# Optimization experiments

Measured on AMD Instinct MI355X. Metric: run time of the kernel, lower is better.

## Reference

```python
import math
import jax, jax.numpy as jnp
import numpy as np

B, T, D, H = 4, 2048, 1024, 16
DH = D // H


def setup_inputs() -> dict:
    key = jax.random.key(0)
    ks = jax.random.split(key, 12)
    s = 1.0 / math.sqrt(D)
    return {
        "query": jax.random.normal(ks[0], (B, T, D), jnp.float32),
        "key": jax.random.normal(ks[1], (B, T, D), jnp.float32),
        "value": jax.random.normal(ks[2], (B, T, D), jnp.float32),
        "mask": jax.random.randint(ks[3], (1, 1, T, T), 0, 2).astype(jnp.bool_),
        "Wq": jax.random.normal(ks[4], (D, D), jnp.float32) * s,
        "bq": jnp.zeros((D,), jnp.float32),
        "Wk": jax.random.normal(ks[5], (D, D), jnp.float32) * s,
        "bk": jnp.zeros((D,), jnp.float32),
        "Wv": jax.random.normal(ks[6], (D, D), jnp.float32) * s,
        "bv": jnp.zeros((D,), jnp.float32),
        "Wo": jax.random.normal(ks[7], (D, D), jnp.float32) * s,
        "bo": jnp.zeros((D,), jnp.float32),
    }


def _heads(x):
    # [B,T,D] -> [B,H,T,DH]
    b, t, _ = x.shape
    return x.reshape(b, t, H, DH).transpose(0, 2, 1, 3)


def reference(query, key, value, mask, Wq, bq, Wk, bk, Wv, bv, Wo, bo):
    q = _heads(query @ Wq.T + bq)
    k = _heads(key @ Wk.T + bk)
    v = _heads(value @ Wv.T + bv)
    # NOTE: original scales by 1/sqrt(embed_dim), not head_dim
    logits = jnp.einsum('bhqd,bhkd->bhqk', q, k) / math.sqrt(D)
    logits = jnp.where(mask, -jnp.inf, logits)
    scores = jax.nn.softmax(logits, axis=-1)
    o = jnp.einsum('bhqk,bhkd->bhqd', scores, v)  # [B,H,T,DH]
    o = o.transpose(0, 2, 1, 3).reshape(query.shape[0], -1, D)
    return o @ Wo.T + bo
```

## Files before the change

kernel.cpp:

```cpp
#include <hip/hip_runtime.h>
#include <hip/hip_bf16.h>

#define D_MODEL 1024
#define SEQ     2048
#define BATCH   4
#define NH      16
#define DHEAD   64

typedef __attribute__((ext_vector_type(8))) short bhalf8;
typedef __attribute__((ext_vector_type(4))) float floatx4;
typedef __attribute__((ext_vector_type(16))) float floatx16;
typedef __attribute__((ext_vector_type(4))) unsigned int uintx4;
typedef __attribute__((ext_vector_type(2))) unsigned int uintx2;

__device__ __forceinline__ void gload16(const void* g, void* l) {
  __builtin_amdgcn_global_load_lds(
      (const __attribute__((address_space(1))) unsigned int*)g,
      (__attribute__((address_space(3))) unsigned int*)l, 16, 0, 0);
}

__device__ __forceinline__ unsigned short f2bf(float x) {
  __hip_bfloat16 h = __float2bfloat16(x);
  return __builtin_bit_cast(unsigned short, h);
}

__device__ __forceinline__ uintx2 pl32(unsigned int a, unsigned int b) {
  return __builtin_amdgcn_permlane32_swap(a, b, false, false);
}

__global__ void cvt_bf16_kernel(const float* __restrict__ in,
                                unsigned short* __restrict__ out, int n4) {
  int i = blockIdx.x * blockDim.x + threadIdx.x;
  if (i >= n4) return;
  float4 v = ((const float4*)in)[i];
  ushort4 o;
  o.x = f2bf(v.x); o.y = f2bf(v.y); o.z = f2bf(v.z); o.w = f2bf(v.w);
  ((ushort4*)out)[i] = o;
}

__global__ void cvt_all_kernel(const float* __restrict__ q, const float* __restrict__ k,
                               const float* __restrict__ v, const float* __restrict__ wq,
                               const float* __restrict__ wk, const float* __restrict__ wv,
                               const float* __restrict__ wo,
                               unsigned short* __restrict__ xq, unsigned short* __restrict__ xk,
                               unsigned short* __restrict__ xv, unsigned short* __restrict__ wqb,
                               unsigned short* __restrict__ wkb, unsigned short* __restrict__ wvb,
                               unsigned short* __restrict__ wob) {
  const int L = blockIdx.x;
  const float* src;
  unsigned short* dst;
  int base;
  if      (L < 8192)  { src = q;  dst = xq;  base = 0; }
  else if (L < 16384) { src = k;  dst = xk;  base = 8192; }
  else if (L < 24576) { src = v;  dst = xv;  base = 16384; }
  else if (L < 25600) { src = wq; dst = wqb; base = 24576; }
  else if (L < 26624) { src = wk; dst = wkb; base = 25600; }
  else if (L < 27648) { src = wv; dst = wvb; base = 26624; }
  else                { src = wo; dst = wob; base = 27648; }
  const int i = (L - base) * 256 + threadIdx.x;
  float4 vv = ((const float4*)src)[i];
  ushort4 o;
  o.x = f2bf(vv.x); o.y = f2bf(vv.y); o.z = f2bf(vv.z); o.w = f2bf(vv.w);
  ((ushort4*)dst)[i] = o;
}

__global__ void detect_mask_kernel(const unsigned int* __restrict__ m,
                                   unsigned int* __restrict__ flag) {
  __shared__ unsigned int not_int, not_flt;
  if (threadIdx.x == 0) { not_int = 0u; not_flt = 0u; }
  __syncthreads();
  unsigned int ni = 0u, nf = 0u;
  for (int j = 0; j < 4; ++j) {
    unsigned int w = m[threadIdx.x * 4 + j];
    if (w > 1u) ni = 1u;
    if (w != 0u && w != 0x3f800000u) nf = 1u;
  }
  if (ni) atomicOr(&not_int, 1u);
  if (nf) atomicOr(&not_flt, 1u);
  __syncthreads();
  if (threadIdx.x == 0) {
    unsigned int f = 1u;
    if (!not_int) f = 0u;
    else if (!not_flt) f = 2u;
    *flag = f;
  }
}

__global__ void pack_mask_kernel(const void* __restrict__ mraw,
                                 const unsigned int* __restrict__ flag,
                                 unsigned long long* __restrict__ bits) {
  int t = blockIdx.x * blockDim.x + threadIdx.x;
  unsigned int f = *flag;
  int v;
  if (f == 1u) v = (((const unsigned char*)mraw)[t] != 0);
  else         v = (((const unsigned int*)mraw)[t] != 0u);
  unsigned long long b = __ballot(v == 0);
  if ((threadIdx.x & 63) == 0) bits[t >> 6] = b;
}

template <int F32OUT>
__device__ __forceinline__ void gemm_core(const unsigned short* __restrict__ A,
                                          const unsigned short* __restrict__ B,
                                          const float* __restrict__ bias,
                                          void* __restrict__ Cout,
                                          int N, float scale, int biasM, int L) {
  __shared__ unsigned short As[2][128][64];
  __shared__ unsigned short Bs[2][128][64];
  const int tid = threadIdx.x;
  const int wid = tid >> 6, lane = tid & 63;
  const int g = lane >> 4, c = lane & 15;
  const int wr = wid >> 1, wc = wid & 1;

  const int xcd = L & 7;
  const int i5 = L >> 3;
  const int u = i5 & 7, v5 = i5 >> 3;
  int bx, by;
  if ((N >> 7) == 8) { bx = u; by = xcd + 8 * v5; }
  else               { bx = xcd + 8 * u; by = v5; }
  const int m0 = by * 128, n0 = bx * 128;

  const floatx4 zero4 = {0.f, 0.f, 0.f, 0.f};
  floatx4 acc[4][4];
#pragma unroll
  for (int i = 0; i < 4; ++i)
#pragma unroll
    for (int j = 0; j < 4; ++j) acc[i][j] = zero4;

  const int r_ = tid >> 3;
  const int sb = ((tid & 7) * 16) ^ (((tid >> 3) & 7) << 4);
  const char* Asrc = (const char*)(A + (size_t)(m0 + r_) * 1024) + sb;
  const char* Bsrc = (const char*)(B + (size_t)(n0 + r_) * 1024) + sb;
  const size_t ROWP = (size_t)32 * 1024 * 2;

  auto stage = [&](int kt, int buf) {
    const size_t ko = (size_t)kt * 128;
#pragma unroll
    for (int p = 0; p < 4; ++p) {
      gload16(Asrc + ko + p * ROWP, (char*)&As[buf][0][0] + p * 4096 + tid * 16);
      gload16(Bsrc + ko + p * ROWP, (char*)&Bs[buf][0][0] + p * 4096 + tid * 16);
    }
  };

  stage(0, 0);
  __syncthreads();
  int cur = 0;
  for (int kt = 0; kt < 16; ++kt) {
    if (kt + 1 < 16) stage(kt + 1, cur ^ 1);
    const char* abase = (const char*)&As[cur][0][0];
    const char* bbase = (const char*)&Bs[cur][0][0];
    bhalf8 a[2][4], b[2][4];
#pragma unroll
    for (int kk = 0; kk < 2; ++kk) {
#pragma unroll
      for (int i = 0; i < 4; ++i) {
        const int row = wr * 64 + i * 16 + c;
        a[kk][i] = *(const bhalf8*)(abase + row * 128 +
                                    ((kk * 64 + g * 16) ^ ((row & 7) << 4)));
      }
#pragma unroll
      for (int j = 0; j < 4; ++j) {
        const int row = wc * 64 + j * 16 + c;
        b[kk][j] = *(const bhalf8*)(bbase + row * 128 +
                                    ((kk * 64 + g * 16) ^ ((row & 7) << 4)));
      }
    }
#pragma unroll
    for (int kk = 0; kk < 2; ++kk)
#pragma unroll
      for (int i = 0; i < 4; ++i)
#pragma unroll
        for (int j = 0; j < 4; ++j)
          acc[i][j] = __builtin_amdgcn_mfma_f32_16x16x32_bf16(a[kk][i], b[kk][j], acc[i][j], 0, 0, 0);
    __syncthreads();
    cur ^= 1;
  }

  float bn[4] = {0.f, 0.f, 0.f, 0.f};
  if (!biasM) {
#pragma unroll
    for (int j = 0; j < 4; ++j) bn[j] = bias[n0 + wc * 64 + j * 16 + c];
  }
#pragma unroll
  for (int i = 0; i < 4; ++i) {
    float bm[4] = {0.f, 0.f, 0.f, 0.f};
    if (biasM) {
#pragma unroll
      for (int r = 0; r < 4; ++r) bm[r] = bias[m0 + wr * 64 + i * 16 + 4 * g + r];
    }
#pragma unroll
    for (int j = 0; j < 4; ++j) {
#pragma unroll
      for (int r = 0; r < 4; ++r) {
        const int m = m0 + wr * 64 + i * 16 + 4 * g + r;
        const int n = n0 + wc * 64 + j * 16 + c;
        const float v = (acc[i][j][r] + (biasM ? bm[r] : bn[j])) * scale;
        if (F32OUT) ((float*)Cout)[(size_t)m * N + n] = v;
        else ((unsigned short*)Cout)[(size_t)m * N + n] = f2bf(v);
      }
    }
  }
}

__global__ __launch_bounds__(256, 2)
void gemm_qkv_kernel(const unsigned short* __restrict__ Xq,
                     const unsigned short* __restrict__ Xk,
                     const unsigned short* __restrict__ Xv,
                     const unsigned short* __restrict__ Wqb,
                     const unsigned short* __restrict__ Wkb,
                     const unsigned short* __restrict__ Wvb,
                     const float* __restrict__ bq, const float* __restrict__ bk,
                     const float* __restrict__ bv,
                     unsigned short* __restrict__ Qb, unsigned short* __restrict__ Kb,
                     unsigned short* __restrict__ Vtb, float qscale, int jsel) {
  int j, L;
  if (jsel == 3) { j = blockIdx.x >> 9; L = blockIdx.x & 511; }
  else           { j = jsel; L = blockIdx.x; }
  const unsigned short* A = (j == 0) ? Xq : (j == 1) ? Xk : Wvb;
  const unsigned short* B = (j == 0) ? Wqb : (j == 1) ? Wkb : Xv;
  const float* bias = (j == 0) ? bq : (j == 1) ? bk : bv;
  unsigned short* C = (j == 0) ? Qb : (j == 1) ? Kb : Vtb;
  const int N = (j == 2) ? 8192 : 1024;
  const float scale = (j == 0) ? qscale : 1.0f;
  gemm_core<0>(A, B, bias, C, N, scale, (j == 2) ? 1 : 0, L);
}

__global__ __launch_bounds__(256, 2)
void gemm_out_kernel(const unsigned short* __restrict__ A,
                     const unsigned short* __restrict__ B,
                     const float* __restrict__ bias, float* __restrict__ C) {
  gemm_core<1>(A, B, bias, C, 1024, 1.0f, 0, blockIdx.x);
}

__global__ __launch_bounds__(256, 3)
void attn_kernel(const unsigned short* __restrict__ Q,
                 const unsigned short* __restrict__ Kmat,
                 const unsigned short* __restrict__ Vt,
                 const unsigned long long* __restrict__ mbits,
                 unsigned short* __restrict__ O) {
  __shared__ unsigned short Ks[2][64][64];
  __shared__ unsigned short Vs[2][64][64];

  const int tid = threadIdx.x;
  const int wid = tid >> 6, lane = tid & 63;
  const int ql = lane & 31;
  const int hi = lane >> 5;

  const int L = blockIdx.x;
  const int xcd = L & 7;
  const int s = L >> 3;
  const int bh = (s & 7) * 8 + xcd;
  const int qt = s >> 3;
  const int b = bh >> 4, h = bh & 15;
  const int q0 = qt * 128 + wid * 32;

  const unsigned short* Qb = Q + (size_t)(b * SEQ + q0) * D_MODEL + h * DHEAD;
  const unsigned short* Kb = Kmat + (size_t)(b * SEQ) * D_MODEL + h * DHEAD;
  const unsigned short* Vb = Vt + (size_t)(h * DHEAD) * (BATCH * SEQ) + (size_t)b * SEQ;

  bhalf8 qf[4];
#pragma unroll
  for (int ks = 0; ks < 4; ++ks)
    qf[ks] = *(const bhalf8*)(Qb + (size_t)ql * D_MODEL + ks * 16 + hi * 8);

  const floatx16 z16 = {0,0,0,0,0,0,0,0,0,0,0,0,0,0,0,0};
  floatx16 ot[2];
  ot[0] = z16; ot[1] = z16;
  floatx16 lt = z16;

  const short ONEB = (short)0x3F80;
  const bhalf8 ones8 = {ONEB, ONEB, ONEB, ONEB, ONEB, ONEB, ONEB, ONEB};

  int koff[4];
#pragma unroll
  for (int ks = 0; ks < 4; ++ks)
    koff[ks] = ql * 128 + ((ks * 32 + hi * 16) ^ ((ql & 7) << 4));

  const int sr = tid >> 3;
  const int sbz = ((tid & 7) * 16) ^ ((sr & 7) << 4);
  const char* Ksrc = (const char*)(Kb + (size_t)sr * D_MODEL) + sbz;
  const char* Vsrc = (const char*)(Vb + (size_t)sr * (BATCH * SEQ)) + sbz;
  const size_t KR32 = (size_t)32 * D_MODEL * 2;
  const size_t VR32 = (size_t)32 * (BATCH * SEQ) * 2;
  const size_t KSTEP = (size_t)64 * D_MODEL * 2;
  const size_t VSTEP = 128;

  const int NT = SEQ / 64;
  gload16(Ksrc,        (char*)&Ks[0][0][0] + tid * 16);
  gload16(Ksrc + KR32, (char*)&Ks[0][0][0] + 4096 + tid * 16);
  gload16(Vsrc,        (char*)&Vs[0][0][0] + tid * 16);
  gload16(Vsrc + VR32, (char*)&Vs[0][0][0] + 4096 + tid * 16);
  __syncthreads();
  const char* kp = Ksrc + KSTEP;
  const char* vp = Vsrc + VSTEP;
  const unsigned long long* mp = mbits + (size_t)(q0 + ql) * (SEQ / 64);
  int cur = 0;

  for (int kt = 0; kt < NT; ++kt) {
    if (kt + 1 < NT) {
      gload16(kp,        (char*)&Ks[cur ^ 1][0][0] + tid * 16);
      gload16(kp + KR32, (char*)&Ks[cur ^ 1][0][0] + 4096 + tid * 16);
      gload16(vp,        (char*)&Vs[cur ^ 1][0][0] + tid * 16);
      gload16(vp + VR32, (char*)&Vs[cur ^ 1][0][0] + 4096 + tid * 16);
      kp += KSTEP;
      vp += VSTEP;
    }
    const unsigned long long mws = mp[kt] >> (4 * hi);
    const unsigned int mlo = (unsigned int)mws;
    const unsigned int mhi32 = (unsigned int)(mws >> 32);

    const char* kbase = (const char*)&Ks[cur][0][0];
    const char* vbase = (const char*)&Vs[cur][0][0];

    floatx16 st[2];
    __builtin_amdgcn_s_setprio(1);
#pragma unroll
    for (int blk = 0; blk < 2; ++blk) {
      const bhalf8 kf0 = *(const bhalf8*)(kbase + koff[0] + blk * 4096);
      st[blk] = __builtin_amdgcn_mfma_f32_32x32x16_bf16(kf0, qf[0], z16, 0, 0, 0);
    }
#pragma unroll
    for (int ks = 1; ks < 4; ++ks) {
#pragma unroll
      for (int blk = 0; blk < 2; ++blk) {
        const bhalf8 kf = *(const bhalf8*)(kbase + koff[ks] + blk * 4096);
        st[blk] = __builtin_amdgcn_mfma_f32_32x32x16_bf16(kf, qf[ks], st[blk], 0, 0, 0);
      }
    }
    __builtin_amdgcn_s_setprio(0);

    unsigned int w[2][8];
#pragma unroll
    for (int blk = 0; blk < 2; ++blk) {
      const unsigned int word = blk ? mhi32 : mlo;
#pragma unroll
      for (int i = 0; i < 8; ++i) {
        const int r0 = 2 * i, r1 = 2 * i + 1;
        const int c0 = (r0 & 3) + 8 * (r0 >> 2);
        const int c1 = c0 + 1;
        float p0 = __builtin_amdgcn_exp2f(st[blk][r0]);
        float p1 = __builtin_amdgcn_exp2f(st[blk][r1]);
        const unsigned int e0 = (unsigned int)__builtin_amdgcn_sbfe((int)word, c0, 1);
        const unsigned int e1 = (unsigned int)__builtin_amdgcn_sbfe((int)word, c1, 1);
        p0 = __builtin_bit_cast(float, __builtin_bit_cast(unsigned int, p0) & e0);
        p1 = __builtin_bit_cast(float, __builtin_bit_cast(unsigned int, p1) & e1);
        w[blk][i] = ((unsigned int)f2bf(p1) << 16) | (unsigned int)f2bf(p0);
      }
    }

    __builtin_amdgcn_s_setprio(1);
#pragma unroll
    for (int blk = 0; blk < 2; ++blk)
#pragma unroll
      for (int s2 = 0; s2 < 2; ++s2) {
        const int ks = blk * 2 + s2;
        const int o = s2 * 4;
        const uintx2 u2 = pl32(w[blk][o + 0], w[blk][o + 2]);
        const uintx2 v2 = pl32(w[blk][o + 1], w[blk][o + 3]);
        uintx4 awv;
        awv[0] = u2[0];  awv[1] = v2[0];  awv[2] = u2[1];  awv[3] = v2[1];
        const bhalf8 pa = __builtin_bit_cast(bhalf8, awv);
#pragma unroll
        for (int db = 0; db < 2; ++db) {
          const bhalf8 vf = *(const bhalf8*)(vbase + koff[ks] + db * 4096);
          ot[db] = __builtin_amdgcn_mfma_f32_32x32x16_bf16(pa, vf, ot[db], 0, 0, 0);
        }
        lt = __builtin_amdgcn_mfma_f32_32x32x16_bf16(pa, ones8, lt, 0, 0, 0);
      }
    __builtin_amdgcn_s_setprio(0);

    __syncthreads();
    cur ^= 1;
  }

#pragma unroll
  for (int r = 0; r < 16; ++r) {
    const int qr = (r & 3) + 8 * (r >> 2) + 4 * hi;
    const float fi = 1.f / lt[r];
    unsigned short* orow = O + (size_t)(b * SEQ + q0 + qr) * D_MODEL + h * DHEAD + ql;
    orow[0]  = f2bf(ot[0][r] * fi);
    orow[32] = f2bf(ot[1][r] * fi);
  }
}

extern "C" void kernel_launch(void* const* d_in, const int* in_sizes, int n_in,
                              void* d_out, int out_size, void* d_ws, size_t ws_size,
                              hipStream_t stream) {
  (void)in_sizes; (void)n_in; (void)out_size;
  const float* query = (const float*)d_in[0];
  const float* key   = (const float*)d_in[1];
  const float* value = (const float*)d_in[2];
  const void*  mask  = d_in[3];
  const float* Wq = (const float*)d_in[4];
  const float* bq = (const float*)d_in[5];
  const float* Wk = (const float*)d_in[6];
  const float* bk = (const float*)d_in[7];
  const float* Wv = (const float*)d_in[8];
  const float* bv = (const float*)d_in[9];
  const float* Wo = (const float*)d_in[10];
  const float* bo = (const float*)d_in[11];

  const float QSCALE = 1.4426950408889634f / 32.0f;
  const size_t XB = (size_t)8192 * 1024 * 2;
  const size_t WB = (size_t)1024 * 1024 * 2;
  const size_t MB = (size_t)2048 * 32 * 8;

  char* ws = (char*)d_ws;
  size_t off = 0;
  auto alloc = [&](size_t bytes) {
    char* p = ws + off;
    off += (bytes + 255) & ~(size_t)255;
    return p;
  };

  {
    size_t o2 = 0;
    auto need = [&](size_t b) { o2 += (b + 255) & ~(size_t)255; };
    need(XB); need(XB); need(XB);
    need(WB); need(WB); need(WB); need(WB);
    need(XB); need(XB); need(XB);
    need(MB); need(256);
    if (o2 <= ws_size) {
      unsigned short* Xq  = (unsigned short*)alloc(XB);
      unsigned short* Xk  = (unsigned short*)alloc(XB);
      unsigned short* Xv  = (unsigned short*)alloc(XB);
      unsigned short* Wqb = (unsigned short*)alloc(WB);
      unsigned short* Wkb = (unsigned short*)alloc(WB);
      unsigned short* Wvb = (unsigned short*)alloc(WB);
      unsigned short* Wob = (unsigned short*)alloc(WB);
      unsigned short* Qb  = (unsigned short*)alloc(XB);
      unsigned short* Kbf = (unsigned short*)alloc(XB);
      unsigned short* Vtb = (unsigned short*)alloc(XB);
      unsigned long long* mbits = (unsigned long long*)alloc(MB);
      unsigned int* flag = (unsigned int*)alloc(256);
      unsigned short* Ob = Xq;

      detect_mask_kernel<<<1, 256, 0, stream>>>((const unsigned int*)mask, flag);
      pack_mask_kernel<<<(SEQ * SEQ) / 256, 256, 0, stream>>>(mask, flag, mbits);
      cvt_all_kernel<<<28672, 256, 0, stream>>>(query, key, value, Wq, Wk, Wv, Wo,
                                                Xq, Xk, Xv, Wqb, Wkb, Wvb, Wob);
      gemm_qkv_kernel<<<1536, 256, 0, stream>>>(Xq, Xk, Xv, Wqb, Wkb, Wvb,
                                                bq, bk, bv, Qb, Kbf, Vtb, QSCALE, 3);
      attn_kernel<<<1024, 256, 0, stream>>>(Qb, Kbf, Vtb, mbits, Ob);
      gemm_out_kernel<<<512, 256, 0, stream>>>(Ob, Wob, bo, (float*)d_out);
      return;
    }
  }

  unsigned short* Xb  = (unsigned short*)alloc(XB);
  unsigned short* Wb  = (unsigned short*)alloc(WB);
  unsigned short* Qb  = (unsigned short*)alloc(XB);
  unsigned short* Kbf = (unsigned short*)alloc(XB);
  unsigned short* Vtb = (unsigned short*)alloc(XB);
  unsigned short* Ob  = (unsigned short*)alloc(XB);
  unsigned long long* mbits = (unsigned long long*)alloc(MB);
  unsigned int* flag = (unsigned int*)alloc(256);
  if (off > ws_size) return;

  detect_mask_kernel<<<1, 256, 0, stream>>>((const unsigned int*)mask, flag);
  pack_mask_kernel<<<(SEQ * SEQ) / 256, 256, 0, stream>>>(mask, flag, mbits);

  cvt_bf16_kernel<<<8192, 256, 0, stream>>>(query, Xb, 2097152);
  cvt_bf16_kernel<<<1024, 256, 0, stream>>>(Wq, Wb, 262144);
  gemm_qkv_kernel<<<512, 256, 0, stream>>>(Xb, Xb, Xb, Wb, Wb, Wb, bq, bk, bv,
                                           Qb, Kbf, Vtb, QSCALE, 0);
  cvt_bf16_kernel<<<8192, 256, 0, stream>>>(key, Xb, 2097152);
  cvt_bf16_kernel<<<1024, 256, 0, stream>>>(Wk, Wb, 262144);
  gemm_qkv_kernel<<<512, 256, 0, stream>>>(Xb, Xb, Xb, Wb, Wb, Wb, bq, bk, bv,
                                           Qb, Kbf, Vtb, QSCALE, 1);
  cvt_bf16_kernel<<<8192, 256, 0, stream>>>(value, Xb, 2097152);
  cvt_bf16_kernel<<<1024, 256, 0, stream>>>(Wv, Wb, 262144);
  gemm_qkv_kernel<<<512, 256, 0, stream>>>(Xb, Xb, Xb, Wb, Wb, Wb, bq, bk, bv,
                                           Qb, Kbf, Vtb, QSCALE, 2);
  attn_kernel<<<1024, 256, 0, stream>>>(Qb, Kbf, Vtb, mbits, Ob);
  cvt_bf16_kernel<<<1024, 256, 0, stream>>>(Wo, Wb, 262144);
  gemm_out_kernel<<<512, 256, 0, stream>>>(Ob, Wb, bo, (float*)d_out);
}
```

Measured before the change: 241.4 us.

## Enlarge attention block to 256 queries, widen conversion and mask packing per thread

The attention kernel now runs 512 threads (8 waves) per block over 256 query rows, so each K/V tile loaded into shared memory is shared by twice as many queries, and each thread issues one async load per tile instead of two. The grid shrinks to 512 blocks. The fp32-to-bf16 conversion kernel handles 8 elements per thread with 16-byte stores, and mask packing produces 8 ballot words per wave, which cuts launch and block overhead. The risks are lower occupancy, since 512 blocks gives fewer waves in flight per CU, and tail imbalance in the attention kernel.

```diff
diff --git a/kernel.cpp b/kernel.cpp
--- a/kernel.cpp
+++ b/kernel.cpp
@@ -12,6 +12,7 @@
 typedef __attribute__((ext_vector_type(16))) float floatx16;
 typedef __attribute__((ext_vector_type(4))) unsigned int uintx4;
 typedef __attribute__((ext_vector_type(2))) unsigned int uintx2;
+typedef __attribute__((ext_vector_type(8))) unsigned short ushort8v;
 
 __device__ __forceinline__ void gload16(const void* g, void* l) {
   __builtin_amdgcn_global_load_lds(
@@ -50,18 +51,20 @@
   const float* src;
   unsigned short* dst;
   int base;
-  if      (L < 8192)  { src = q;  dst = xq;  base = 0; }
-  else if (L < 16384) { src = k;  dst = xk;  base = 8192; }
-  else if (L < 24576) { src = v;  dst = xv;  base = 16384; }
-  else if (L < 25600) { src = wq; dst = wqb; base = 24576; }
-  else if (L < 26624) { src = wk; dst = wkb; base = 25600; }
-  else if (L < 27648) { src = wv; dst = wvb; base = 26624; }
-  else                { src = wo; dst = wob; base = 27648; }
+  if      (L < 4096)  { src = q;  dst = xq;  base = 0; }
+  else if (L < 8192)  { src = k;  dst = xk;  base = 4096; }
+  else if (L < 12288) { src = v;  dst = xv;  base = 8192; }
+  else if (L < 12800) { src = wq; dst = wqb; base = 12288; }
+  else if (L < 13312) { src = wk; dst = wkb; base = 12800; }
+  else if (L < 13824) { src = wv; dst = wvb; base = 13312; }
+  else                { src = wo; dst = wob; base = 13824; }
   const int i = (L - base) * 256 + threadIdx.x;
-  float4 vv = ((const float4*)src)[i];
-  ushort4 o;
-  o.x = f2bf(vv.x); o.y = f2bf(vv.y); o.z = f2bf(vv.z); o.w = f2bf(vv.w);
-  ((ushort4*)dst)[i] = o;
+  const float4 v0 = ((const float4*)src)[2 * i];
+  const float4 v1 = ((const float4*)src)[2 * i + 1];
+  ushort8v o;
+  o[0] = f2bf(v0.x); o[1] = f2bf(v0.y); o[2] = f2bf(v0.z); o[3] = f2bf(v0.w);
+  o[4] = f2bf(v1.x); o[5] = f2bf(v1.y); o[6] = f2bf(v1.z); o[7] = f2bf(v1.w);
+  ((ushort8v*)dst)[i] = o;
 }
 
 __global__ void detect_mask_kernel(const unsigned int* __restrict__ m,
@@ -89,13 +92,18 @@
 __global__ void pack_mask_kernel(const void* __restrict__ mraw,
                                  const unsigned int* __restrict__ flag,
                                  unsigned long long* __restrict__ bits) {
-  int t = blockIdx.x * blockDim.x + threadIdx.x;
-  unsigned int f = *flag;
-  int v;
-  if (f == 1u) v = (((const unsigned char*)mraw)[t] != 0);
-  else         v = (((const unsigned int*)mraw)[t] != 0u);
-  unsigned long long b = __ballot(v == 0);
-  if ((threadIdx.x & 63) == 0) bits[t >> 6] = b;
+  const unsigned int f = *flag;
+  const int lane = threadIdx.x & 63;
+  const int w0 = ((blockIdx.x * blockDim.x + threadIdx.x) >> 6) * 8;
+#pragma unroll
+  for (int e = 0; e < 8; ++e) {
+    const int t = (w0 + e) * 64 + lane;
+    int v;
+    if (f == 1u) v = (((const unsigned char*)mraw)[t] != 0);
+    else         v = (((const unsigned int*)mraw)[t] != 0u);
+    const unsigned long long b = __ballot(v == 0);
+    if (lane == 0) bits[w0 + e] = b;
+  }
 }
 
 template <int F32OUT>
@@ -231,7 +239,7 @@
   gemm_core<1>(A, B, bias, C, 1024, 1.0f, 0, blockIdx.x);
 }
 
-__global__ __launch_bounds__(256, 3)
+__global__ __launch_bounds__(512, 2)
 void attn_kernel(const unsigned short* __restrict__ Q,
                  const unsigned short* __restrict__ Kmat,
                  const unsigned short* __restrict__ Vt,
@@ -251,7 +259,7 @@
   const int bh = (s & 7) * 8 + xcd;
   const int qt = s >> 3;
   const int b = bh >> 4, h = bh & 15;
-  const int q0 = qt * 128 + wid * 32;
+  const int q0 = qt * 256 + wid * 32;
 
   const unsigned short* Qb = Q + (size_t)(b * SEQ + q0) * D_MODEL + h * DHEAD;
   const unsigned short* Kb = Kmat + (size_t)(b * SEQ) * D_MODEL + h * DHEAD;
@@ -279,16 +287,12 @@
   const int sbz = ((tid & 7) * 16) ^ ((sr & 7) << 4);
   const char* Ksrc = (const char*)(Kb + (size_t)sr * D_MODEL) + sbz;
   const char* Vsrc = (const char*)(Vb + (size_t)sr * (BATCH * SEQ)) + sbz;
-  const size_t KR32 = (size_t)32 * D_MODEL * 2;
-  const size_t VR32 = (size_t)32 * (BATCH * SEQ) * 2;
   const size_t KSTEP = (size_t)64 * D_MODEL * 2;
   const size_t VSTEP = 128;
 
   const int NT = SEQ / 64;
-  gload16(Ksrc,        (char*)&Ks[0][0][0] + tid * 16);
-  gload16(Ksrc + KR32, (char*)&Ks[0][0][0] + 4096 + tid * 16);
-  gload16(Vsrc,        (char*)&Vs[0][0][0] + tid * 16);
-  gload16(Vsrc + VR32, (char*)&Vs[0][0][0] + 4096 + tid * 16);
+  gload16(Ksrc, (char*)&Ks[0][0][0] + tid * 16);
+  gload16(Vsrc, (char*)&Vs[0][0][0] + tid * 16);
   __syncthreads();
   const char* kp = Ksrc + KSTEP;
   const char* vp = Vsrc + VSTEP;
@@ -297,10 +301,8 @@
 
   for (int kt = 0; kt < NT; ++kt) {
     if (kt + 1 < NT) {
-      gload16(kp,        (char*)&Ks[cur ^ 1][0][0] + tid * 16);
-      gload16(kp + KR32, (char*)&Ks[cur ^ 1][0][0] + 4096 + tid * 16);
-      gload16(vp,        (char*)&Vs[cur ^ 1][0][0] + tid * 16);
-      gload16(vp + VR32, (char*)&Vs[cur ^ 1][0][0] + 4096 + tid * 16);
+      gload16(kp, (char*)&Ks[cur ^ 1][0][0] + tid * 16);
+      gload16(vp, (char*)&Vs[cur ^ 1][0][0] + tid * 16);
       kp += KSTEP;
       vp += VSTEP;
     }
@@ -435,12 +437,12 @@
       unsigned short* Ob = Xq;
 
       detect_mask_kernel<<<1, 256, 0, stream>>>((const unsigned int*)mask, flag);
-      pack_mask_kernel<<<(SEQ * SEQ) / 256, 256, 0, stream>>>(mask, flag, mbits);
-      cvt_all_kernel<<<28672, 256, 0, stream>>>(query, key, value, Wq, Wk, Wv, Wo,
+      pack_mask_kernel<<<2048, 256, 0, stream>>>(mask, flag, mbits);
+      cvt_all_kernel<<<14336, 256, 0, stream>>>(query, key, value, Wq, Wk, Wv, Wo,
                                                 Xq, Xk, Xv, Wqb, Wkb, Wvb, Wob);
       gemm_qkv_kernel<<<1536, 256, 0, stream>>>(Xq, Xk, Xv, Wqb, Wkb, Wvb,
                                                 bq, bk, bv, Qb, Kbf, Vtb, QSCALE, 3);
-      attn_kernel<<<1024, 256, 0, stream>>>(Qb, Kbf, Vtb, mbits, Ob);
+      attn_kernel<<<512, 512, 0, stream>>>(Qb, Kbf, Vtb, mbits, Ob);
       gemm_out_kernel<<<512, 256, 0, stream>>>(Ob, Wob, bo, (float*)d_out);
       return;
     }
@@ -457,7 +459,7 @@
   if (off > ws_size) return;
 
   detect_mask_kernel<<<1, 256, 0, stream>>>((const unsigned int*)mask, flag);
-  pack_mask_kernel<<<(SEQ * SEQ) / 256, 256, 0, stream>>>(mask, flag, mbits);
+  pack_mask_kernel<<<2048, 256, 0, stream>>>(mask, flag, mbits);
 
   cvt_bf16_kernel<<<8192, 256, 0, stream>>>(query, Xb, 2097152);
   cvt_bf16_kernel<<<1024, 256, 0, stream>>>(Wq, Wb, 262144);
@@ -471,7 +473,7 @@
   cvt_bf16_kernel<<<1024, 256, 0, stream>>>(Wv, Wb, 262144);
   gemm_qkv_kernel<<<512, 256, 0, stream>>>(Xb, Xb, Xb, Wb, Wb, Wb, bq, bk, bv,
                                            Qb, Kbf, Vtb, QSCALE, 2);
-  attn_kernel<<<1024, 256, 0, stream>>>(Qb, Kbf, Vtb, mbits, Ob);
+  attn_kernel<<<512, 512, 0, stream>>>(Qb, Kbf, Vtb, mbits, Ob);
   cvt_bf16_kernel<<<1024, 256, 0, stream>>>(Wo, Wb, 262144);
   gemm_out_kernel<<<512, 256, 0, stream>>>(Ob, Wb, bo, (float*)d_out);
 }
```

Result: faster. 232.2 us, median of 2 (-3.8%).
